# Performance work log

Measured on AMD Instinct MI355X. Metric: run time of the kernel, lower is better.

The kernel has to match this reference:

```python
import jax, jax.numpy as jnp
import numpy as np

C_SKIP = 64       # channels of a and of b (concat -> 128)
C_OUT = 64
N = 131072        # coarse nodes
E = 1048576       # directed edges (avg degree 8)
N_FINE = 4 * N    # fine mesh nodes after unpool
K = 3 * N_FINE    # unpool scatter assignments


def setup_inputs() -> dict:
    key = jax.random.key(0)
    ks = jax.random.split(key, 9)
    return {
        "a": jax.random.normal(ks[0], (C_SKIP, N), dtype=jnp.float32),
        "b": jax.random.normal(ks[1], (C_SKIP, N), dtype=jnp.float32),
        "W_self": jax.random.normal(ks[2], (C_OUT, 2 * C_SKIP), dtype=jnp.float32) * 0.05,
        "W_neigh": jax.random.normal(ks[3], (C_OUT, 2 * C_SKIP), dtype=jnp.float32) * 0.05,
        "bias": jax.random.normal(ks[4], (C_OUT,), dtype=jnp.float32) * 0.05,
        "gather_index": jax.random.randint(ks[5], (E,), 0, N),
        "reduce_index": jax.random.randint(ks[6], (E,), 0, N),
        "unpool_src": jax.random.randint(ks[7], (K,), 0, N),
        "unpool_dst": jax.random.randint(ks[8], (K,), 0, N_FINE),
    }


def reference(a, b, W_self, W_neigh, bias, gather_index, reduce_index, unpool_src, unpool_dst):
    # concat skip connection along channel dim (-2)
    x = jnp.concatenate((a, b), axis=-2)                  # [C_in, N]
    n = x.shape[-1]
    # GraphConv: gather source features along edges, segment-sum into targets
    msgs = x[:, gather_index]                              # [C_in, E]
    agg = jax.ops.segment_sum(msgs.T, reduce_index, num_segments=n).T  # [C_in, N]
    h = W_self @ x + W_neigh @ agg + bias[:, None]         # [C_out, N]
    h = jax.nn.relu(h)
    # GraphUnpool with reduce='amax': scatter-max coarse features to fine mesh
    out = jnp.zeros((h.shape[0], 4 * n), dtype=h.dtype)
    out = out.at[:, unpool_dst].max(h[:, unpool_src])      # [C_out, N_fine]
    return out
```

## Files before the change

kernel.cpp:

```cpp
#include <hip/hip_runtime.h>
#include <stdint.h>

constexpr int NN = 131072;
constexpr int EE = 1048576;
constexpr int NF = 4 * NN;
constexpr int KK = 3 * NF;

constexpr int NSB  = 256;
constexpr int TPS  = 1024;
constexpr int SHC_E = 9;
constexpr int SHC_K = 10;
constexpr int NBC_E = NN >> SHC_E;
constexpr int NBC_K = NF >> SHC_K;
constexpr int EPT_E = EE / NSB / TPS;
constexpr int EPT_K = KK / NSB / TPS;
constexpr int KOFF2 = NBC_E * NSB;
constexpr int NH2   = KOFF2 + NBC_K * NSB;
constexpr int NSCB  = NH2 / 2048;
constexpr int NTRB  = NN / 32 / 4;

constexpr int CAP3_E = 5120;
constexpr int CAP3_K = 4096;

typedef __attribute__((ext_vector_type(8))) short bf16x8;
typedef __attribute__((ext_vector_type(4))) float f32x4;

__device__ inline uint32_t bf16rn(float f) {
    uint32_t u = __float_as_uint(f);
    return (u + 0x7FFFu + ((u >> 16) & 1u)) >> 16;
}
__device__ inline uint32_t pack2(float lo, float hi) {
    return bf16rn(lo) | (bf16rn(hi) << 16);
}
__device__ inline float bf_lo(uint32_t v) { return __uint_as_float(v << 16); }
__device__ inline float bf_hi(uint32_t v) { return __uint_as_float(v & 0xFFFF0000u); }

template<int NB, int EPT>
__device__ void pass1_body(const int* __restrict__ idx, int shift,
                           int* __restrict__ histG, int blk, int* hist)
{
    for (int f = threadIdx.x; f < NB; f += TPS) hist[f] = 0;
    __syncthreads();
    int base = blk * (TPS * EPT);
#pragma unroll
    for (int u = 0; u < EPT; ++u) {
        int b = idx[base + u * TPS + threadIdx.x] >> shift;
        atomicAdd(&hist[b], 1);
    }
    __syncthreads();
    for (int f = threadIdx.x; f < NB; f += TPS)
        histG[f * NSB + blk] = hist[f];
}

__global__ __launch_bounds__(1024) void k_fused1(
    const float* __restrict__ a, const float* __restrict__ b,
    uint32_t* __restrict__ xTb,
    const int* __restrict__ reduce_i, const int* __restrict__ up_dst,
    int* __restrict__ histG)
{
    __shared__ int smem[128 * 33];
    if (blockIdx.x < NTRB) {
        float (*tile)[33] = (float (*)[33])smem;
        for (int t = 0; t < 4; ++t) {
            int i0 = (blockIdx.x * 4 + t) * 32;
            for (int f = threadIdx.x; f < 128 * 32; f += TPS) {
                int c = f >> 5, j = f & 31;
                const float* src = (c < 64) ? a : b;
                tile[c][j] = src[(size_t)(c & 63) * NN + i0 + j];
            }
            __syncthreads();
            for (int f = threadIdx.x; f < 64 * 32; f += TPS) {
                int p = f & 63, j = f >> 6;
                xTb[(size_t)(i0 + j) * 64 + p] =
                    pack2(tile[2 * p][j], tile[2 * p + 1][j]);
            }
            __syncthreads();
        }
    } else if (blockIdx.x < NTRB + NSB) {
        pass1_body<NBC_E, EPT_E>(reduce_i, SHC_E, histG, blockIdx.x - NTRB, smem);
    } else {
        pass1_body<NBC_K, EPT_K>(up_dst, SHC_K, histG + KOFF2,
                                 blockIdx.x - NTRB - NSB, smem);
    }
}

__global__ __launch_bounds__(256) void k_bsum(
    const int* __restrict__ cnt, int* __restrict__ bsum)
{
    __shared__ int s[256];
    int base = blockIdx.x * 2048;
    int sum = 0;
    for (int j = threadIdx.x; j < 2048; j += 256) sum += cnt[base + j];
    s[threadIdx.x] = sum;
    __syncthreads();
    for (int o = 128; o > 0; o >>= 1) {
        if (threadIdx.x < o) s[threadIdx.x] += s[threadIdx.x + o];
        __syncthreads();
    }
    if (threadIdx.x == 0) bsum[blockIdx.x] = s[0];
}

__global__ __launch_bounds__(256) void k_final(
    int* __restrict__ offs, const int* __restrict__ bsum)
{
    __shared__ int ts[256];
    int partial = 0;
    for (int i = threadIdx.x; i < blockIdx.x; i += 256) partial += bsum[i];
    ts[threadIdx.x] = partial;
    __syncthreads();
    for (int o = 128; o > 0; o >>= 1) {
        if (threadIdx.x < o) ts[threadIdx.x] += ts[threadIdx.x + o];
        __syncthreads();
    }
    int bb = ts[0];
    __syncthreads();

    int base = blockIdx.x * 2048 + threadIdx.x * 8;
    int loc[8];
    int sum = 0;
#pragma unroll
    for (int u = 0; u < 8; ++u) {
        int v = offs[base + u];
        loc[u] = sum;
        sum += v;
    }
    ts[threadIdx.x] = sum;
    __syncthreads();
    for (int o = 1; o < 256; o <<= 1) {
        int v = (threadIdx.x >= o) ? ts[threadIdx.x - o] : 0;
        __syncthreads();
        ts[threadIdx.x] += v;
        __syncthreads();
    }
    int texc = (threadIdx.x == 0) ? 0 : ts[threadIdx.x - 1];
#pragma unroll
    for (int u = 0; u < 8; ++u) offs[base + u] = bb + texc + loc[u];
    if (blockIdx.x == gridDim.x - 1 && threadIdx.x == 255) offs[NH2] = bb + ts[255];
}

template<int NB, int EPT>
__device__ void pass2_body(const int* __restrict__ idx,
                           const int* __restrict__ payload, int shift,
                           const int* __restrict__ offsG, int sub,
                           uint32_t* __restrict__ pairs, int blk, int* curs)
{
    int lmask = (1 << shift) - 1;
    for (int f = threadIdx.x; f < NB; f += TPS)
        curs[f] = offsG[f * NSB + blk] - sub;
    __syncthreads();
    int base = blk * (TPS * EPT);
#pragma unroll
    for (int u = 0; u < EPT; ++u) {
        int e = base + u * TPS + threadIdx.x;
        int bk = idx[e];
        int pos = atomicAdd(&curs[bk >> shift], 1);
        pairs[pos] = (uint32_t)payload[e] | ((uint32_t)(bk & lmask) << 17);
    }
}

__global__ __launch_bounds__(1024) void k_pass2(
    const int* __restrict__ reduce_i, const int* __restrict__ gather_i,
    const int* __restrict__ up_dst, const int* __restrict__ up_src,
    const int* __restrict__ offs,
    uint32_t* __restrict__ pairsE, uint32_t* __restrict__ pairsK)
{
    __shared__ int curs[NBC_K];
    if (blockIdx.x < NSB)
        pass2_body<NBC_E, EPT_E>(reduce_i, gather_i, SHC_E, offs, 0,
                                 pairsE, blockIdx.x, curs);
    else
        pass2_body<NBC_K, EPT_K>(up_dst, up_src, SHC_K, offs + KOFF2, EE,
                                 pairsK, blockIdx.x - NSB, curs);
}

template<int NB, int CAP>
__device__ void pass3_body(uint32_t* __restrict__ pairs, int beg, int end,
                           int* __restrict__ nodeOff, int nodeBase,
                           bool last, int totalNode,
                           uint32_t* list, int* curs, int* tmp)
{
    int tid = threadIdx.x;
    int cnt = min(end - beg, CAP);
    for (int i = tid; i < cnt; i += TPS) list[i] = pairs[beg + i];
    if (tid < NB) curs[tid] = 0;
    __syncthreads();
    for (int i = tid; i < cnt; i += TPS) atomicAdd(&curs[list[i] >> 17], 1);
    __syncthreads();
    int own = (tid < NB) ? curs[tid] : 0;
    if (tid < NB) tmp[tid] = own;
    __syncthreads();
    for (int o = 1; o < NB; o <<= 1) {
        int v = (tid < NB && tid >= o) ? tmp[tid - o] : 0;
        __syncthreads();
        if (tid < NB) tmp[tid] += v;
        __syncthreads();
    }
    if (tid < NB) {
        int excl = tmp[tid] - own;
        curs[tid] = excl;
        nodeOff[nodeBase + tid] = beg + excl;
    }
    if (last && tid == 0) nodeOff[totalNode] = beg + cnt;
    __syncthreads();
    for (int i = tid; i < cnt; i += TPS) {
        uint32_t u = list[i];
        int p = atomicAdd(&curs[u >> 17], 1);
        pairs[beg + p] = u;
    }
}

__global__ __launch_bounds__(1024) void k_pass3(
    const int* __restrict__ offs,
    uint32_t* __restrict__ pairsE, uint32_t* __restrict__ pairsK,
    int* __restrict__ nodeOffE, int* __restrict__ nodeOffK)
{
    __shared__ uint32_t list[CAP3_E];
    __shared__ int curs[1024];
    __shared__ int tmp[1024];
    if (blockIdx.x < NBC_E) {
        int b = blockIdx.x;
        int beg = offs[b * NSB], end = offs[(b + 1) * NSB];
        pass3_body<512, CAP3_E>(pairsE, beg, end, nodeOffE, b * 512,
                                b == NBC_E - 1, NN, list, curs, tmp);
    } else {
        int b = blockIdx.x - NBC_E;
        int beg = offs[KOFF2 + b * NSB] - EE;
        int end = offs[KOFF2 + (b + 1) * NSB] - EE;
        pass3_body<1024, CAP3_K>(pairsK, beg, end, nodeOffK, b * 1024,
                                 b == NBC_K - 1, NF, list, curs, tmp);
    }
}

__global__ __launch_bounds__(256) void k_agg2(
    const uint32_t* __restrict__ xTb, const int* __restrict__ nodeOffE,
    const uint32_t* __restrict__ pairsE, uint32_t* __restrict__ aggB)
{
    int w = threadIdx.x >> 6, lane = threadIdx.x & 63;
    int n0g = blockIdx.x * 64 + w * 16;
    int e0 = nodeOffE[n0g], e1 = nodeOffE[n0g + 16];
    int curLoc = n0g & 511;
    int curEnd = curLoc + 16;
    int cbase = n0g - curLoc;
    float sx = 0.f, sy = 0.f;
    int cur = curLoc;
    for (int e = e0; e < e1; e += 16) {
        int nb = e1 - e;
        uint32_t pr[16], v[16];
#pragma unroll
        for (int j = 0; j < 16; ++j)
            pr[j] = pairsE[e + ((j < nb) ? j : (nb - 1))];
#pragma unroll
        for (int j = 0; j < 16; ++j)
            v[j] = xTb[(size_t)(pr[j] & 0x1FFFF) * 64 + lane];
#pragma unroll
        for (int j = 0; j < 16; ++j) {
            if (j < nb) {
                int d = pr[j] >> 17;
                if (d != cur) {
                    aggB[(size_t)(cbase + cur) * 64 + lane] = pack2(sx, sy);
                    for (int z = cur + 1; z < d; ++z)
                        aggB[(size_t)(cbase + z) * 64 + lane] = 0u;
                    cur = d;
                    sx = 0.f; sy = 0.f;
                }
                sx += bf_lo(v[j]);
                sy += bf_hi(v[j]);
            }
        }
    }
    aggB[(size_t)(cbase + cur) * 64 + lane] = pack2(sx, sy);
    for (int z = cur + 1; z < curEnd; ++z)
        aggB[(size_t)(cbase + z) * 64 + lane] = 0u;
}

__global__ __launch_bounds__(256) void k_gemm(
    const uint32_t* __restrict__ xTb, const uint32_t* __restrict__ aggB,
    const float* __restrict__ Wself, const float* __restrict__ Wneigh,
    const float* __restrict__ bias, uint32_t* __restrict__ hT)
{
    int lane = threadIdx.x & 63;
    int wid = blockIdx.x * 4 + (threadIdx.x >> 6);
    int lr = lane & 15, lq = lane >> 4;

    bf16x8 wf[4][8];
#pragma unroll
    for (int mt = 0; mt < 4; ++mt) {
#pragma unroll
        for (int kt = 0; kt < 8; ++kt) {
            const float* W = (kt < 4) ? Wself : Wneigh;
            const float* p = W + (size_t)(mt * 16 + lr) * 128 + (kt & 3) * 32 + lq * 8;
            bf16x8 v;
#pragma unroll
            for (int j = 0; j < 8; ++j) v[j] = (short)bf16rn(p[j]);
            wf[mt][kt] = v;
        }
    }
    float bv[4][4];
#pragma unroll
    for (int mt = 0; mt < 4; ++mt)
#pragma unroll
        for (int r = 0; r < 4; ++r)
            bv[mt][r] = bias[mt * 16 + lq * 4 + r];

    const int NG = NN / 16;
    int stride = gridDim.x * 4;
    for (int g = wid; g < NG; g += stride) {
        int n = g * 16 + lr;
        const uint32_t* xr = xTb + (size_t)n * 64 + lq * 4;
        const uint32_t* ar = aggB + (size_t)n * 64 + lq * 4;
        bf16x8 bq[8];
#pragma unroll
        for (int kt = 0; kt < 4; ++kt)
            bq[kt] = *reinterpret_cast<const bf16x8*>(xr + kt * 16);
#pragma unroll
        for (int kt = 0; kt < 4; ++kt)
            bq[4 + kt] = *reinterpret_cast<const bf16x8*>(ar + kt * 16);
#pragma unroll
        for (int mt = 0; mt < 4; ++mt) {
            f32x4 acc = {0.f, 0.f, 0.f, 0.f};
#pragma unroll
            for (int kt = 0; kt < 8; ++kt)
                acc = __builtin_amdgcn_mfma_f32_16x16x32_bf16(wf[mt][kt], bq[kt], acc, 0, 0, 0);
            uint32_t u0 = pack2(fmaxf(acc[0] + bv[mt][0], 0.f), fmaxf(acc[1] + bv[mt][1], 0.f));
            uint32_t u1 = pack2(fmaxf(acc[2] + bv[mt][2], 0.f), fmaxf(acc[3] + bv[mt][3], 0.f));
            *reinterpret_cast<uint2*>(hT + (size_t)n * 32 + mt * 8 + lq * 2) = make_uint2(u0, u1);
        }
    }
}

__global__ __launch_bounds__(256) void k_unpool2(
    const uint16_t* __restrict__ hT16, const int* __restrict__ nodeOffK,
    const uint32_t* __restrict__ pairsK, float* __restrict__ out)
{
    __shared__ uint16_t buf[128][65];
    int w = threadIdx.x >> 6, lane = threadIdx.x & 63;
    int j0 = blockIdx.x * 128;
    int lbase = j0 & 1023;
    for (int f = threadIdx.x; f < 128 * 65; f += 256) ((uint16_t*)buf)[f] = 0;
    __syncthreads();
    int n0 = j0 + w * 32;
    int e0 = nodeOffK[n0], e1 = nodeOffK[n0 + 32];
    uint32_t m = 0;
    int cur = (n0 & 1023) - lbase;
    for (int e = e0; e < e1; e += 16) {
        int nb = e1 - e;
        uint32_t pr[16], v[16];
#pragma unroll
        for (int j = 0; j < 16; ++j)
            pr[j] = pairsK[e + ((j < nb) ? j : (nb - 1))];
#pragma unroll
        for (int j = 0; j < 16; ++j)
            v[j] = hT16[(size_t)(pr[j] & 0x1FFFF) * 64 + lane];
#pragma unroll
        for (int j = 0; j < 16; ++j) {
            if (j < nb) {
                int d = (int)(pr[j] >> 17) - lbase;
                if (d != cur) {
                    buf[cur][lane] = (uint16_t)m;
                    cur = d;
                    m = 0;
                }
                m = max(m, v[j]);
            }
        }
    }
    buf[cur][lane] = (uint16_t)m;
    __syncthreads();
    for (int f = threadIdx.x; f < 64 * 128; f += 256) {
        int c = f >> 7, j = f & 127;
        out[(size_t)c * NF + j0 + j] = __uint_as_float(((uint32_t)buf[j][c]) << 16);
    }
}

extern "C" void kernel_launch(void* const* d_in, const int* in_sizes, int n_in,
                              void* d_out, int out_size, void* d_ws, size_t ws_size,
                              hipStream_t stream)
{
    const float* a      = (const float*)d_in[0];
    const float* b      = (const float*)d_in[1];
    const float* Wself  = (const float*)d_in[2];
    const float* Wneigh = (const float*)d_in[3];
    const float* bias   = (const float*)d_in[4];
    const int* gather_i = (const int*)d_in[5];
    const int* reduce_i = (const int*)d_in[6];
    const int* up_src   = (const int*)d_in[7];
    const int* up_dst   = (const int*)d_in[8];
    float* out = (float*)d_out;

    uint32_t* xTb    = (uint32_t*)d_ws;
    uint32_t* aggB   = xTb + (size_t)NN * 64;
    uint32_t* hT     = aggB + (size_t)NN * 64;
    uint32_t* pairsK = hT + (size_t)NN * 32;
    int* offs        = (int*)(pairsK + KK);
    int* bsum        = offs + (size_t)NH2 + 1;
    int* nodeOffE    = bsum + NSCB;
    int* nodeOffK    = nodeOffE + NN + 1;
    uint32_t* pairsE = hT;

    size_t need = ((size_t)NN * 160 + KK + (size_t)NH2 + 1 + NSCB +
                   (size_t)NN + 1 + (size_t)NF + 1) * 4;
    if (ws_size < need) return;

    k_fused1<<<NTRB + 2 * NSB, TPS, 0, stream>>>(a, b, xTb, reduce_i, up_dst, offs);

    k_bsum<<<NSCB, 256, 0, stream>>>(offs, bsum);
    k_final<<<NSCB, 256, 0, stream>>>(offs, bsum);

    k_pass2<<<2 * NSB, TPS, 0, stream>>>(reduce_i, gather_i, up_dst, up_src,
                                         offs, pairsE, pairsK);

    k_pass3<<<NBC_E + NBC_K, TPS, 0, stream>>>(offs, pairsE, pairsK,
                                               nodeOffE, nodeOffK);

    k_agg2<<<NN / 64, 256, 0, stream>>>(xTb, nodeOffE, pairsE, aggB);

    k_gemm<<<512, 256, 0, stream>>>(xTb, aggB, Wself, Wneigh, bias, hT);

    k_unpool2<<<NF / 128, 256, 0, stream>>>((const uint16_t*)hT, nodeOffK,
                                            pairsK, out);
}
```

Before: 245.6 us.

## Fuse per-bucket local sort into aggregation and unpool kernels

The separate pass3 kernel, which sorted each coarse bucket and wrote node offsets to global memory, is removed. Its local counting sort now runs inside the aggregation and unpool kernels, with the sorted list kept in shared memory, so a launch and the global write and re-read of the pairs and node offsets go away. The edge bucket width drops from 512 to 256 nodes so each aggregation block covers one bucket with 1024 threads, and the transpose load now uses float4 reads. The cost is fewer, larger blocks: 512 blocks for aggregation, and 512 blocks for unpool that each loop over eight 128-node chunks with block barriers between them.

```diff
diff --git a/kernel.cpp b/kernel.cpp
--- a/kernel.cpp
+++ b/kernel.cpp
@@ -8,7 +8,7 @@
 
 constexpr int NSB  = 256;
 constexpr int TPS  = 1024;
-constexpr int SHC_E = 9;
+constexpr int SHC_E = 8;
 constexpr int SHC_K = 10;
 constexpr int NBC_E = NN >> SHC_E;
 constexpr int NBC_K = NF >> SHC_K;
@@ -19,7 +19,7 @@
 constexpr int NSCB  = NH2 / 2048;
 constexpr int NTRB  = NN / 32 / 4;
 
-constexpr int CAP3_E = 5120;
+constexpr int CAP3_E = 2560;
 constexpr int CAP3_K = 4096;
 
 typedef __attribute__((ext_vector_type(8))) short bf16x8;
@@ -63,10 +63,14 @@
         float (*tile)[33] = (float (*)[33])smem;
         for (int t = 0; t < 4; ++t) {
             int i0 = (blockIdx.x * 4 + t) * 32;
-            for (int f = threadIdx.x; f < 128 * 32; f += TPS) {
-                int c = f >> 5, j = f & 31;
+            {
+                int f = threadIdx.x;
+                int c = f >> 3, j4 = (f & 7) << 2;
                 const float* src = (c < 64) ? a : b;
-                tile[c][j] = src[(size_t)(c & 63) * NN + i0 + j];
+                float4 v = *reinterpret_cast<const float4*>(
+                    src + (size_t)(c & 63) * NN + i0 + j4);
+                tile[c][j4] = v.x; tile[c][j4 + 1] = v.y;
+                tile[c][j4 + 2] = v.z; tile[c][j4 + 3] = v.w;
             }
             __syncthreads();
             for (int f = threadIdx.x; f < 64 * 32; f += TPS) {
@@ -164,7 +168,7 @@
     const int* __restrict__ offs,
     uint32_t* __restrict__ pairsE, uint32_t* __restrict__ pairsK)
 {
-    __shared__ int curs[NBC_K];
+    __shared__ int curs[512];
     if (blockIdx.x < NSB)
         pass2_body<NBC_E, EPT_E>(reduce_i, gather_i, SHC_E, offs, 0,
                                  pairsE, blockIdx.x, curs);
@@ -173,82 +177,57 @@
                                  pairsK, blockIdx.x - NSB, curs);
 }
 
-template<int NB, int CAP>
-__device__ void pass3_body(uint32_t* __restrict__ pairs, int beg, int end,
-                           int* __restrict__ nodeOff, int nodeBase,
-                           bool last, int totalNode,
-                           uint32_t* list, int* curs, int* tmp)
-{
+__global__ __launch_bounds__(1024) void k_agg3(
+    const uint32_t* __restrict__ xTb, const int* __restrict__ offs,
+    const uint32_t* __restrict__ pairsE, uint32_t* __restrict__ aggB)
+{
+    __shared__ uint32_t list[CAP3_E];
+    __shared__ uint32_t list2[CAP3_E];
+    __shared__ int curs[256], tmp[256];
+    __shared__ int loffs[257];
     int tid = threadIdx.x;
-    int cnt = min(end - beg, CAP);
-    for (int i = tid; i < cnt; i += TPS) list[i] = pairs[beg + i];
-    if (tid < NB) curs[tid] = 0;
+    int b = blockIdx.x;
+    int beg = offs[b * NSB], end = offs[(b + 1) * NSB];
+    int cnt = min(end - beg, CAP3_E);
+    for (int i = tid; i < cnt; i += TPS) list[i] = pairsE[beg + i];
+    if (tid < 256) curs[tid] = 0;
     __syncthreads();
     for (int i = tid; i < cnt; i += TPS) atomicAdd(&curs[list[i] >> 17], 1);
     __syncthreads();
-    int own = (tid < NB) ? curs[tid] : 0;
-    if (tid < NB) tmp[tid] = own;
-    __syncthreads();
-    for (int o = 1; o < NB; o <<= 1) {
-        int v = (tid < NB && tid >= o) ? tmp[tid - o] : 0;
-        __syncthreads();
-        if (tid < NB) tmp[tid] += v;
-        __syncthreads();
-    }
-    if (tid < NB) {
-        int excl = tmp[tid] - own;
+    if (tid < 256) tmp[tid] = curs[tid];
+    __syncthreads();
+    for (int o = 1; o < 256; o <<= 1) {
+        int v = (tid < 256 && tid >= o) ? tmp[tid - o] : 0;
+        __syncthreads();
+        if (tid < 256) tmp[tid] += v;
+        __syncthreads();
+    }
+    if (tid < 256) {
+        int excl = tmp[tid] - curs[tid];
+        loffs[tid] = excl;
         curs[tid] = excl;
-        nodeOff[nodeBase + tid] = beg + excl;
-    }
-    if (last && tid == 0) nodeOff[totalNode] = beg + cnt;
+    }
+    if (tid == 0) loffs[256] = cnt;
     __syncthreads();
     for (int i = tid; i < cnt; i += TPS) {
         uint32_t u = list[i];
         int p = atomicAdd(&curs[u >> 17], 1);
-        pairs[beg + p] = u;
-    }
-}
-
-__global__ __launch_bounds__(1024) void k_pass3(
-    const int* __restrict__ offs,
-    uint32_t* __restrict__ pairsE, uint32_t* __restrict__ pairsK,
-    int* __restrict__ nodeOffE, int* __restrict__ nodeOffK)
-{
-    __shared__ uint32_t list[CAP3_E];
-    __shared__ int curs[1024];
-    __shared__ int tmp[1024];
-    if (blockIdx.x < NBC_E) {
-        int b = blockIdx.x;
-        int beg = offs[b * NSB], end = offs[(b + 1) * NSB];
-        pass3_body<512, CAP3_E>(pairsE, beg, end, nodeOffE, b * 512,
-                                b == NBC_E - 1, NN, list, curs, tmp);
-    } else {
-        int b = blockIdx.x - NBC_E;
-        int beg = offs[KOFF2 + b * NSB] - EE;
-        int end = offs[KOFF2 + (b + 1) * NSB] - EE;
-        pass3_body<1024, CAP3_K>(pairsK, beg, end, nodeOffK, b * 1024,
-                                 b == NBC_K - 1, NF, list, curs, tmp);
-    }
-}
-
-__global__ __launch_bounds__(256) void k_agg2(
-    const uint32_t* __restrict__ xTb, const int* __restrict__ nodeOffE,
-    const uint32_t* __restrict__ pairsE, uint32_t* __restrict__ aggB)
-{
-    int w = threadIdx.x >> 6, lane = threadIdx.x & 63;
-    int n0g = blockIdx.x * 64 + w * 16;
-    int e0 = nodeOffE[n0g], e1 = nodeOffE[n0g + 16];
-    int curLoc = n0g & 511;
-    int curEnd = curLoc + 16;
-    int cbase = n0g - curLoc;
+        list2[p] = u;
+    }
+    __syncthreads();
+
+    int w = tid >> 6, lane = tid & 63;
+    int n0 = w * 16, n1 = n0 + 16;
+    int e0 = loffs[n0], e1 = loffs[n1];
+    int cbase = b * 256;
     float sx = 0.f, sy = 0.f;
-    int cur = curLoc;
+    int cur = n0;
     for (int e = e0; e < e1; e += 16) {
         int nb = e1 - e;
         uint32_t pr[16], v[16];
 #pragma unroll
         for (int j = 0; j < 16; ++j)
-            pr[j] = pairsE[e + ((j < nb) ? j : (nb - 1))];
+            pr[j] = list2[e + ((j < nb) ? j : (nb - 1))];
 #pragma unroll
         for (int j = 0; j < 16; ++j)
             v[j] = xTb[(size_t)(pr[j] & 0x1FFFF) * 64 + lane];
@@ -269,7 +248,7 @@
         }
     }
     aggB[(size_t)(cbase + cur) * 64 + lane] = pack2(sx, sy);
-    for (int z = cur + 1; z < curEnd; ++z)
+    for (int z = cur + 1; z < n1; ++z)
         aggB[(size_t)(cbase + z) * 64 + lane] = 0u;
 }
 
@@ -328,47 +307,85 @@
     }
 }
 
-__global__ __launch_bounds__(256) void k_unpool2(
-    const uint16_t* __restrict__ hT16, const int* __restrict__ nodeOffK,
+__global__ __launch_bounds__(1024) void k_unpool3(
+    const uint16_t* __restrict__ hT16, const int* __restrict__ offsK,
     const uint32_t* __restrict__ pairsK, float* __restrict__ out)
 {
+    __shared__ uint32_t list[CAP3_K];
+    __shared__ uint32_t list2[CAP3_K];
+    __shared__ int curs[1024], tmp[1024];
+    __shared__ int loffs[1025];
     __shared__ uint16_t buf[128][65];
-    int w = threadIdx.x >> 6, lane = threadIdx.x & 63;
-    int j0 = blockIdx.x * 128;
-    int lbase = j0 & 1023;
-    for (int f = threadIdx.x; f < 128 * 65; f += 256) ((uint16_t*)buf)[f] = 0;
-    __syncthreads();
-    int n0 = j0 + w * 32;
-    int e0 = nodeOffK[n0], e1 = nodeOffK[n0 + 32];
-    uint32_t m = 0;
-    int cur = (n0 & 1023) - lbase;
-    for (int e = e0; e < e1; e += 16) {
-        int nb = e1 - e;
-        uint32_t pr[16], v[16];
-#pragma unroll
-        for (int j = 0; j < 16; ++j)
-            pr[j] = pairsK[e + ((j < nb) ? j : (nb - 1))];
-#pragma unroll
-        for (int j = 0; j < 16; ++j)
-            v[j] = hT16[(size_t)(pr[j] & 0x1FFFF) * 64 + lane];
-#pragma unroll
-        for (int j = 0; j < 16; ++j) {
-            if (j < nb) {
-                int d = (int)(pr[j] >> 17) - lbase;
-                if (d != cur) {
-                    buf[cur][lane] = (uint16_t)m;
-                    cur = d;
-                    m = 0;
+    int tid = threadIdx.x;
+    int b = blockIdx.x;
+    int beg = offsK[b * NSB] - EE, end = offsK[(b + 1) * NSB] - EE;
+    int cnt = min(end - beg, CAP3_K);
+    for (int i = tid; i < cnt; i += TPS) list[i] = pairsK[beg + i];
+    curs[tid] = 0;
+    __syncthreads();
+    for (int i = tid; i < cnt; i += TPS) atomicAdd(&curs[list[i] >> 17], 1);
+    __syncthreads();
+    tmp[tid] = curs[tid];
+    __syncthreads();
+    for (int o = 1; o < 1024; o <<= 1) {
+        int v = (tid >= o) ? tmp[tid - o] : 0;
+        __syncthreads();
+        tmp[tid] += v;
+        __syncthreads();
+    }
+    {
+        int excl = tmp[tid] - curs[tid];
+        loffs[tid] = excl;
+        curs[tid] = excl;
+    }
+    if (tid == 0) loffs[1024] = cnt;
+    __syncthreads();
+    for (int i = tid; i < cnt; i += TPS) {
+        uint32_t u = list[i];
+        int p = atomicAdd(&curs[u >> 17], 1);
+        list2[p] = u;
+    }
+    __syncthreads();
+
+    int w = tid >> 6, lane = tid & 63;
+    for (int cc = 0; cc < 8; ++cc) {
+        for (int f = tid; f < 128 * 65; f += TPS) ((uint16_t*)buf)[f] = 0;
+        __syncthreads();
+        int n0 = cc * 128 + w * 8;
+        int e0 = loffs[n0], e1 = loffs[n0 + 8];
+        uint32_t m = 0;
+        int cur = w * 8;
+        for (int e = e0; e < e1; e += 16) {
+            int nb = e1 - e;
+            uint32_t pr[16], v[16];
+#pragma unroll
+            for (int j = 0; j < 16; ++j)
+                pr[j] = list2[e + ((j < nb) ? j : (nb - 1))];
+#pragma unroll
+            for (int j = 0; j < 16; ++j)
+                v[j] = hT16[(size_t)(pr[j] & 0x1FFFF) * 64 + lane];
+#pragma unroll
+            for (int j = 0; j < 16; ++j) {
+                if (j < nb) {
+                    int d = (int)(pr[j] >> 17) - cc * 128;
+                    if (d != cur) {
+                        buf[cur][lane] = (uint16_t)m;
+                        cur = d;
+                        m = 0;
+                    }
+                    m = max(m, v[j]);
                 }
-                m = max(m, v[j]);
             }
         }
-    }
-    buf[cur][lane] = (uint16_t)m;
-    __syncthreads();
-    for (int f = threadIdx.x; f < 64 * 128; f += 256) {
-        int c = f >> 7, j = f & 127;
-        out[(size_t)c * NF + j0 + j] = __uint_as_float(((uint32_t)buf[j][c]) << 16);
+        buf[cur][lane] = (uint16_t)m;
+        __syncthreads();
+        int j0 = b * 1024 + cc * 128;
+        for (int f = tid; f < 64 * 128; f += TPS) {
+            int c = f >> 7, j = f & 127;
+            out[(size_t)c * NF + j0 + j] =
+                __uint_as_float(((uint32_t)buf[j][c]) << 16);
+        }
+        __syncthreads();
     }
 }
 
@@ -393,12 +410,9 @@
     uint32_t* pairsK = hT + (size_t)NN * 32;
     int* offs        = (int*)(pairsK + KK);
     int* bsum        = offs + (size_t)NH2 + 1;
-    int* nodeOffE    = bsum + NSCB;
-    int* nodeOffK    = nodeOffE + NN + 1;
     uint32_t* pairsE = hT;
 
-    size_t need = ((size_t)NN * 160 + KK + (size_t)NH2 + 1 + NSCB +
-                   (size_t)NN + 1 + (size_t)NF + 1) * 4;
+    size_t need = ((size_t)NN * 160 + KK + (size_t)NH2 + 1 + NSCB) * 4;
     if (ws_size < need) return;
 
     k_fused1<<<NTRB + 2 * NSB, TPS, 0, stream>>>(a, b, xTb, reduce_i, up_dst, offs);
@@ -409,13 +423,10 @@
     k_pass2<<<2 * NSB, TPS, 0, stream>>>(reduce_i, gather_i, up_dst, up_src,
                                          offs, pairsE, pairsK);
 
-    k_pass3<<<NBC_E + NBC_K, TPS, 0, stream>>>(offs, pairsE, pairsK,
-                                               nodeOffE, nodeOffK);
-
-    k_agg2<<<NN / 64, 256, 0, stream>>>(xTb, nodeOffE, pairsE, aggB);
+    k_agg3<<<NBC_E, TPS, 0, stream>>>(xTb, offs, pairsE, aggB);
 
     k_gemm<<<512, 256, 0, stream>>>(xTb, aggB, Wself, Wneigh, bias, hT);
 
-    k_unpool2<<<NF / 128, 256, 0, stream>>>((const uint16_t*)hT, nodeOffK,
-                                            pairsK, out);
-}
+    k_unpool3<<<NBC_K, TPS, 0, stream>>>((const uint16_t*)hT, offs + KOFF2,
+                                         pairsK, out);
+}
```

After: 246.6 us. Within noise of the previous version (+0.4%).

## Split feature tables into channel slabs for cache-resident gather and unpool

Applied to the files above, without the earlier changes.

Stores the transposed bf16 features, the aggregates and the activations as eight channel slabs of 32 bytes per node instead of 256-byte rows. The aggregation and unpool kernels now have blocks handle one slab for a bucket of nodes, with 8 lanes per node group, so each slab's gather working set is smaller and more likely to stay in cache. The unpool also writes output directly per channel row instead of going through a shared transpose buffer, which makes those stores less coalesced. Alongside this, the edge bucket shift is reduced to match 256-node buckets and the transpose load is vectorised to float4.

```diff
diff --git a/kernel.cpp b/kernel.cpp
--- a/kernel.cpp
+++ b/kernel.cpp
@@ -8,7 +8,7 @@
 
 constexpr int NSB  = 256;
 constexpr int TPS  = 1024;
-constexpr int SHC_E = 9;
+constexpr int SHC_E = 8;
 constexpr int SHC_K = 10;
 constexpr int NBC_E = NN >> SHC_E;
 constexpr int NBC_K = NF >> SHC_K;
@@ -19,7 +19,7 @@
 constexpr int NSCB  = NH2 / 2048;
 constexpr int NTRB  = NN / 32 / 4;
 
-constexpr int CAP3_E = 5120;
+constexpr int CAP3_E = 2560;
 constexpr int CAP3_K = 4096;
 
 typedef __attribute__((ext_vector_type(8))) short bf16x8;
@@ -34,6 +34,7 @@
 }
 __device__ inline float bf_lo(uint32_t v) { return __uint_as_float(v << 16); }
 __device__ inline float bf_hi(uint32_t v) { return __uint_as_float(v & 0xFFFF0000u); }
+
 
 template<int NB, int EPT>
 __device__ void pass1_body(const int* __restrict__ idx, int shift,
@@ -63,15 +64,19 @@
         float (*tile)[33] = (float (*)[33])smem;
         for (int t = 0; t < 4; ++t) {
             int i0 = (blockIdx.x * 4 + t) * 32;
-            for (int f = threadIdx.x; f < 128 * 32; f += TPS) {
-                int c = f >> 5, j = f & 31;
+            {
+                int f = threadIdx.x;
+                int c = f >> 3, j4 = (f & 7) << 2;
                 const float* src = (c < 64) ? a : b;
-                tile[c][j] = src[(size_t)(c & 63) * NN + i0 + j];
+                float4 v = *reinterpret_cast<const float4*>(
+                    src + (size_t)(c & 63) * NN + i0 + j4);
+                tile[c][j4] = v.x; tile[c][j4 + 1] = v.y;
+                tile[c][j4 + 2] = v.z; tile[c][j4 + 3] = v.w;
             }
             __syncthreads();
             for (int f = threadIdx.x; f < 64 * 32; f += TPS) {
                 int p = f & 63, j = f >> 6;
-                xTb[(size_t)(i0 + j) * 64 + p] =
+                xTb[(size_t)(p >> 3) * (NN * 8) + (size_t)(i0 + j) * 8 + (p & 7)] =
                     pack2(tile[2 * p][j], tile[2 * p + 1][j]);
             }
             __syncthreads();
@@ -164,7 +169,7 @@
     const int* __restrict__ offs,
     uint32_t* __restrict__ pairsE, uint32_t* __restrict__ pairsK)
 {
-    __shared__ int curs[NBC_K];
+    __shared__ int curs[512];
     if (blockIdx.x < NSB)
         pass2_body<NBC_E, EPT_E>(reduce_i, gather_i, SHC_E, offs, 0,
                                  pairsE, blockIdx.x, curs);
@@ -214,53 +219,54 @@
     uint32_t* __restrict__ pairsE, uint32_t* __restrict__ pairsK,
     int* __restrict__ nodeOffE, int* __restrict__ nodeOffK)
 {
-    __shared__ uint32_t list[CAP3_E];
+    __shared__ uint32_t list[CAP3_K];
     __shared__ int curs[1024];
     __shared__ int tmp[1024];
     if (blockIdx.x < NBC_E) {
         int b = blockIdx.x;
-        int beg = offs[b * NSB], end = offs[(b + 1) * NSB];
-        pass3_body<512, CAP3_E>(pairsE, beg, end, nodeOffE, b * 512,
-                                b == NBC_E - 1, NN, list, curs, tmp);
+        pass3_body<256, CAP3_E>(pairsE, offs[b * NSB], offs[(b + 1) * NSB],
+                                nodeOffE, b * 256, b == NBC_E - 1, NN,
+                                list, curs, tmp);
     } else {
         int b = blockIdx.x - NBC_E;
-        int beg = offs[KOFF2 + b * NSB] - EE;
-        int end = offs[KOFF2 + (b + 1) * NSB] - EE;
-        pass3_body<1024, CAP3_K>(pairsK, beg, end, nodeOffK, b * 1024,
-                                 b == NBC_K - 1, NF, list, curs, tmp);
-    }
-}
-
-__global__ __launch_bounds__(256) void k_agg2(
+        pass3_body<1024, CAP3_K>(pairsK, offs[KOFF2 + b * NSB] - EE,
+                                 offs[KOFF2 + (b + 1) * NSB] - EE,
+                                 nodeOffK, b * 1024, b == NBC_K - 1, NF,
+                                 list, curs, tmp);
+    }
+}
+
+__global__ __launch_bounds__(256) void k_agg4(
     const uint32_t* __restrict__ xTb, const int* __restrict__ nodeOffE,
     const uint32_t* __restrict__ pairsE, uint32_t* __restrict__ aggB)
 {
-    int w = threadIdx.x >> 6, lane = threadIdx.x & 63;
-    int n0g = blockIdx.x * 64 + w * 16;
-    int e0 = nodeOffE[n0g], e1 = nodeOffE[n0g + 16];
-    int curLoc = n0g & 511;
-    int curEnd = curLoc + 16;
-    int cbase = n0g - curLoc;
+    int s = blockIdx.x & 7;
+    int d = blockIdx.x >> 3;
+    int g = threadIdx.x >> 3, k = threadIdx.x & 7;
+    const uint32_t* slab = xTb + (size_t)s * (NN * 8);
+    uint32_t* aslab = aggB + (size_t)s * (NN * 8);
+    int gn0 = d * 256 + g * 8;
+    int e0 = nodeOffE[gn0], e1 = nodeOffE[gn0 + 8];
     float sx = 0.f, sy = 0.f;
-    int cur = curLoc;
-    for (int e = e0; e < e1; e += 16) {
+    int cur = gn0;
+    for (int e = e0; e < e1; e += 8) {
         int nb = e1 - e;
-        uint32_t pr[16], v[16];
-#pragma unroll
-        for (int j = 0; j < 16; ++j)
+        uint32_t pr[8], v[8];
+#pragma unroll
+        for (int j = 0; j < 8; ++j)
             pr[j] = pairsE[e + ((j < nb) ? j : (nb - 1))];
 #pragma unroll
-        for (int j = 0; j < 16; ++j)
-            v[j] = xTb[(size_t)(pr[j] & 0x1FFFF) * 64 + lane];
-#pragma unroll
-        for (int j = 0; j < 16; ++j) {
+        for (int j = 0; j < 8; ++j)
+            v[j] = slab[(size_t)(pr[j] & 0x1FFFF) * 8 + k];
+#pragma unroll
+        for (int j = 0; j < 8; ++j) {
             if (j < nb) {
-                int d = pr[j] >> 17;
-                if (d != cur) {
-                    aggB[(size_t)(cbase + cur) * 64 + lane] = pack2(sx, sy);
-                    for (int z = cur + 1; z < d; ++z)
-                        aggB[(size_t)(cbase + z) * 64 + lane] = 0u;
-                    cur = d;
+                int dn = d * 256 + (int)(pr[j] >> 17);
+                if (dn != cur) {
+                    aslab[(size_t)cur * 8 + k] = pack2(sx, sy);
+                    for (int z = cur + 1; z < dn; ++z)
+                        aslab[(size_t)z * 8 + k] = 0u;
+                    cur = dn;
                     sx = 0.f; sy = 0.f;
                 }
                 sx += bf_lo(v[j]);
@@ -268,9 +274,9 @@
             }
         }
     }
-    aggB[(size_t)(cbase + cur) * 64 + lane] = pack2(sx, sy);
-    for (int z = cur + 1; z < curEnd; ++z)
-        aggB[(size_t)(cbase + z) * 64 + lane] = 0u;
+    aslab[(size_t)cur * 8 + k] = pack2(sx, sy);
+    for (int z = cur + 1; z < gn0 + 8; ++z)
+        aslab[(size_t)z * 8 + k] = 0u;
 }
 
 __global__ __launch_bounds__(256) void k_gemm(
@@ -304,17 +310,17 @@
 
     const int NG = NN / 16;
     int stride = gridDim.x * 4;
+    int sbase = (lq >> 1);
+    int woff = (lq & 1) * 4;
     for (int g = wid; g < NG; g += stride) {
         int n = g * 16 + lr;
-        const uint32_t* xr = xTb + (size_t)n * 64 + lq * 4;
-        const uint32_t* ar = aggB + (size_t)n * 64 + lq * 4;
         bf16x8 bq[8];
 #pragma unroll
-        for (int kt = 0; kt < 4; ++kt)
-            bq[kt] = *reinterpret_cast<const bf16x8*>(xr + kt * 16);
-#pragma unroll
-        for (int kt = 0; kt < 4; ++kt)
-            bq[4 + kt] = *reinterpret_cast<const bf16x8*>(ar + kt * 16);
+        for (int kt = 0; kt < 4; ++kt) {
+            size_t base = (size_t)(kt * 2 + sbase) * (NN * 8) + (size_t)n * 8 + woff;
+            bq[kt]     = *reinterpret_cast<const bf16x8*>(xTb + base);
+            bq[4 + kt] = *reinterpret_cast<const bf16x8*>(aggB + base);
+        }
 #pragma unroll
         for (int mt = 0; mt < 4; ++mt) {
             f32x4 acc = {0.f, 0.f, 0.f, 0.f};
@@ -323,53 +329,51 @@
                 acc = __builtin_amdgcn_mfma_f32_16x16x32_bf16(wf[mt][kt], bq[kt], acc, 0, 0, 0);
             uint32_t u0 = pack2(fmaxf(acc[0] + bv[mt][0], 0.f), fmaxf(acc[1] + bv[mt][1], 0.f));
             uint32_t u1 = pack2(fmaxf(acc[2] + bv[mt][2], 0.f), fmaxf(acc[3] + bv[mt][3], 0.f));
-            *reinterpret_cast<uint2*>(hT + (size_t)n * 32 + mt * 8 + lq * 2) = make_uint2(u0, u1);
-        }
-    }
-}
-
-__global__ __launch_bounds__(256) void k_unpool2(
+            *reinterpret_cast<uint2*>(
+                hT + (size_t)(mt * 2 + sbase) * (NN * 4) + (size_t)n * 4 + (lq & 1) * 2)
+                = make_uint2(u0, u1);
+        }
+    }
+}
+
+__global__ __launch_bounds__(256) void k_unpool4(
     const uint16_t* __restrict__ hT16, const int* __restrict__ nodeOffK,
     const uint32_t* __restrict__ pairsK, float* __restrict__ out)
 {
-    __shared__ uint16_t buf[128][65];
-    int w = threadIdx.x >> 6, lane = threadIdx.x & 63;
-    int j0 = blockIdx.x * 128;
-    int lbase = j0 & 1023;
-    for (int f = threadIdx.x; f < 128 * 65; f += 256) ((uint16_t*)buf)[f] = 0;
-    __syncthreads();
-    int n0 = j0 + w * 32;
-    int e0 = nodeOffK[n0], e1 = nodeOffK[n0 + 32];
+    int s = blockIdx.x & 7;
+    int d = blockIdx.x >> 3;
+    int g = threadIdx.x >> 3, k = threadIdx.x & 7;
+    const uint16_t* slab = hT16 + (size_t)s * (NN * 8);
+    float* orow = out + (size_t)(s * 8 + k) * NF;
+    int gn0 = d * 1024 + g * 32;
+    int e0 = nodeOffK[gn0], e1 = nodeOffK[gn0 + 32];
     uint32_t m = 0;
-    int cur = (n0 & 1023) - lbase;
-    for (int e = e0; e < e1; e += 16) {
+    int cur = gn0;
+    for (int e = e0; e < e1; e += 8) {
         int nb = e1 - e;
-        uint32_t pr[16], v[16];
-#pragma unroll
-        for (int j = 0; j < 16; ++j)
+        uint32_t pr[8], v[8];
+#pragma unroll
+        for (int j = 0; j < 8; ++j)
             pr[j] = pairsK[e + ((j < nb) ? j : (nb - 1))];
 #pragma unroll
-        for (int j = 0; j < 16; ++j)
-            v[j] = hT16[(size_t)(pr[j] & 0x1FFFF) * 64 + lane];
-#pragma unroll
-        for (int j = 0; j < 16; ++j) {
+        for (int j = 0; j < 8; ++j)
+            v[j] = slab[(size_t)(pr[j] & 0x1FFFF) * 8 + k];
+#pragma unroll
+        for (int j = 0; j < 8; ++j) {
             if (j < nb) {
-                int d = (int)(pr[j] >> 17) - lbase;
-                if (d != cur) {
-                    buf[cur][lane] = (uint16_t)m;
-                    cur = d;
+                int dn = d * 1024 + (int)(pr[j] >> 17);
+                if (dn != cur) {
+                    orow[cur] = __uint_as_float(m << 16);
+                    for (int z = cur + 1; z < dn; ++z) orow[z] = 0.f;
+                    cur = dn;
                     m = 0;
                 }
                 m = max(m, v[j]);
             }
         }
     }
-    buf[cur][lane] = (uint16_t)m;
-    __syncthreads();
-    for (int f = threadIdx.x; f < 64 * 128; f += 256) {
-        int c = f >> 7, j = f & 127;
-        out[(size_t)c * NF + j0 + j] = __uint_as_float(((uint32_t)buf[j][c]) << 16);
-    }
+    orow[cur] = __uint_as_float(m << 16);
+    for (int z = cur + 1; z < gn0 + 32; ++z) orow[z] = 0.f;
 }
 
 extern "C" void kernel_launch(void* const* d_in, const int* in_sizes, int n_in,
@@ -412,10 +416,10 @@
     k_pass3<<<NBC_E + NBC_K, TPS, 0, stream>>>(offs, pairsE, pairsK,
                                                nodeOffE, nodeOffK);
 
-    k_agg2<<<NN / 64, 256, 0, stream>>>(xTb, nodeOffE, pairsE, aggB);
+    k_agg4<<<NBC_E * 8, 256, 0, stream>>>(xTb, nodeOffE, pairsE, aggB);
 
     k_gemm<<<512, 256, 0, stream>>>(xTb, aggB, Wself, Wneigh, bias, hT);
 
-    k_unpool2<<<NF / 128, 256, 0, stream>>>((const uint16_t*)hT, nodeOffK,
-                                            pairsK, out);
-}
+    k_unpool4<<<NBC_K * 8, 256, 0, stream>>>((const uint16_t*)hT, nodeOffK,
+                                             pairsK, out);
+}
```

Measured after the change: 634.5 us. +158.4%, slower.
